# Performance work log

Measured on AMD Instinct MI355X. Metric: run time of the kernel, lower is better.

## Reference

```python
import jax, jax.numpy as jnp
import numpy as np

PI = float(np.pi)


def _mat(rows):
    # rows: 4 lists of 4 [..., ] arrays -> [..., 4, 4]
    return jnp.stack([jnp.stack(r, axis=-1) for r in rows], axis=-2)


def _local_frames(q):
    """q: [..., 7] joint angles -> list of 8 local [..., 4, 4] transforms."""
    z = jnp.zeros_like(q[..., 0])
    o = jnp.ones_like(z)

    def cs(a):
        return jnp.cos(a), jnp.sin(a)

    c0, s0 = cs(q[..., 0])
    c1, s1 = cs(q[..., 1])
    c2, s2 = cs(q[..., 2] - 0.5 * PI)
    c3, s3 = cs(q[..., 3])
    c4, s4 = cs(q[..., 4])
    c5, s5 = cs(q[..., 5] + 0.5 * PI)
    c6, s6 = cs(q[..., 6] - 0.5 * PI)

    m0 = _mat([[c0, -s0, z, z], [s0, c0, z, z], [z, z, o, z], [z, z, z, o]])
    m1 = _mat([[c1, -s1, z, z], [z, z, -o, z], [s1, c1, z, z], [z, z, z, o]])
    m2 = _mat([[c2, -s2, z, z], [z, z, o, 0.4 * o], [-s2, -c2, z, z], [z, z, z, o]])
    m3 = _mat([[c3, -s3, z, z], [z, z, -o, z], [s3, c3, z, z], [z, z, z, o]])
    m4 = _mat([[-c4, s4, z, z], [z, z, o, 0.39 * o], [s4, c4, z, z], [z, z, z, o]])
    m5 = _mat([[c5, -s5, z, z], [z, z, -o, z], [s5, c5, z, z], [z, z, z, o]])
    m6 = _mat([[c6, -s6, z, z], [z, z, -o, z], [s6, c6, z, z], [z, z, z, o]])
    m7 = _mat([[-o, z, z, z], [z, z, o, 0.118 * o], [z, o, z, z], [z, z, z, o]])
    return [m0, m1, m2, m3, m4, m5, m6, m7]


def setup_inputs() -> dict:
    key = jax.random.key(0)
    x = jax.random.normal(key, (2000000, 7), dtype=jnp.float32)
    return {"x": x}


def reference(x):
    mats = _local_frames(x)
    frames = [mats[0]]
    f = mats[0]
    for m in mats[1:]:  # fixed chain of 7 tiny 4x4 matmuls over batch
        f = jnp.einsum("...ij,...jk->...ik", f, m)
        frames.append(f)
    return jnp.stack(frames, axis=-3)  # [..., 8, 4, 4]
```

## Files before the change

### kernel.cpp

```cpp
#include <hip/hip_runtime.h>


#define GROUPS_PER_BLOCK 8
#define LSTRIDE 25

namespace {

struct V3 { float x, y, z; };
__device__ __forceinline__ V3 v3(float x, float y, float z) { return {x, y, z}; }

__device__ __forceinline__ void stage3(float4* p, V3 c0, V3 c1, V3 c2, V3 c3) {
    p[0] = make_float4(c0.x, c1.x, c2.x, c3.x);
    p[1] = make_float4(c0.y, c1.y, c2.y, c3.y);
    p[2] = make_float4(c0.z, c1.z, c2.z, c3.z);
}

__device__ __forceinline__ void compute_stage(const float* __restrict__ q,
                                              float4* __restrict__ buf,
                                              int lane, long long grp, long long n)
{
    long long i = grp * 64 + lane;
    if (i >= n) i = n - 1;
    const float* qi = q + i * 7;
    const float HPI = 1.57079632679489662f;

    float qv[7];
    #pragma unroll
    for (int k = 0; k < 7; ++k) qv[k] = qi[k];

    float c[7], s[7];
    __sincosf(qv[0], &s[0], &c[0]);
    __sincosf(qv[1], &s[1], &c[1]);
    __sincosf(qv[2] - HPI, &s[2], &c[2]);
    __sincosf(qv[3], &s[3], &c[3]);
    __sincosf(qv[4], &s[4], &c[4]);
    __sincosf(qv[5] + HPI, &s[5], &c[5]);
    __sincosf(qv[6] - HPI, &s[6], &c[6]);

    float4* myS = buf + lane * LSTRIDE;

    V3 f0 = v3(c[0], s[0], 0.f);
    V3 f1 = v3(-s[0], c[0], 0.f);
    V3 f2 = v3(0.f, 0.f, 1.f);
    V3 f3 = v3(0.f, 0.f, 0.f);

    #define TYPE_A(cc, ss)                                              \
        {                                                               \
            V3 t0 = v3((cc)*f0.x + (ss)*f2.x, (cc)*f0.y + (ss)*f2.y, (cc)*f0.z + (ss)*f2.z); \
            V3 t1 = v3((cc)*f2.x - (ss)*f0.x, (cc)*f2.y - (ss)*f0.y, (cc)*f2.z - (ss)*f0.z); \
            V3 t2 = v3(-f1.x, -f1.y, -f1.z);                            \
            f0 = t0; f1 = t1; f2 = t2;                                  \
        }

    stage3(myS + 0, f0, f1, f2, f3);

    TYPE_A(c[1], s[1]);
    stage3(myS + 3, f0, f1, f2, f3);

    {
        V3 t0 = v3(c[2]*f0.x - s[2]*f2.x, c[2]*f0.y - s[2]*f2.y, c[2]*f0.z - s[2]*f2.z);
        V3 t1 = v3(-(s[2]*f0.x + c[2]*f2.x), -(s[2]*f0.y + c[2]*f2.y), -(s[2]*f0.z + c[2]*f2.z));
        V3 t2 = f1;
        f3 = v3(0.4f*f1.x + f3.x, 0.4f*f1.y + f3.y, 0.4f*f1.z + f3.z);
        f0 = t0; f1 = t1; f2 = t2;
    }
    stage3(myS + 6, f0, f1, f2, f3);

    TYPE_A(c[3], s[3]);
    stage3(myS + 9, f0, f1, f2, f3);

    {
        V3 t0 = v3(s[4]*f2.x - c[4]*f0.x, s[4]*f2.y - c[4]*f0.y, s[4]*f2.z - c[4]*f0.z);
        V3 t1 = v3(s[4]*f0.x + c[4]*f2.x, s[4]*f0.y + c[4]*f2.y, s[4]*f0.z + c[4]*f2.z);
        V3 t2 = f1;
        f3 = v3(0.39f*f1.x + f3.x, 0.39f*f1.y + f3.y, 0.39f*f1.z + f3.z);
        f0 = t0; f1 = t1; f2 = t2;
    }
    stage3(myS + 12, f0, f1, f2, f3);

    TYPE_A(c[5], s[5]);
    stage3(myS + 15, f0, f1, f2, f3);

    TYPE_A(c[6], s[6]);
    stage3(myS + 18, f0, f1, f2, f3);

    {
        V3 t0 = v3(-f0.x, -f0.y, -f0.z);
        V3 t1 = f2;
        V3 t2 = f1;
        f3 = v3(0.118f*f1.x + f3.x, 0.118f*f1.y + f3.y, 0.118f*f1.z + f3.z);
        f0 = t0; f1 = t1; f2 = t2;
    }
    stage3(myS + 21, f0, f1, f2, f3);

    #undef TYPE_A
}

__device__ __forceinline__ void flush_group(const float4* __restrict__ buf,
                                            float4* __restrict__ out,
                                            int lane, long long grp, long long n,
                                            bool full)
{
    const int p  = lane & 31;
    const int eh = lane >> 5;
    const int f  = p >> 2;
    const int r  = p & 3;
    const int rr = (r == 3) ? 2 : r;
    const int base_off = eh * LSTRIDE + f * 3 + rr;
    const bool isr3 = (r == 3);
    float4* gb = out + grp * 2048;

    if (full) {
        #pragma unroll
        for (int j = 0; j < 32; ++j) {
            float4 v = buf[j * (2 * LSTRIDE) + base_off];
            if (isr3) v = make_float4(0.f, 0.f, 0.f, 1.f);
            gb[j * 64 + lane] = v;
        }
    } else {
        #pragma unroll
        for (int j = 0; j < 32; ++j) {
            float4 v = buf[j * (2 * LSTRIDE) + base_off];
            if (isr3) v = make_float4(0.f, 0.f, 0.f, 1.f);
            long long e = (long long)((j * 64 + lane) >> 5);
            if (grp * 64 + e < n) gb[j * 64 + lane] = v;
        }
    }
}

}

__global__ __launch_bounds__(64) void fk_chain_kernel(const float* __restrict__ q,
                                                      float4* __restrict__ out,
                                                      int n, int ngroups)
{
    __shared__ float4 lds[2][64 * LSTRIDE];

    const int lane = threadIdx.x;
    const long long g0 = (long long)blockIdx.x * GROUPS_PER_BLOCK;
    if (g0 >= ngroups) return;
    const int ng = (ngroups - g0 < GROUPS_PER_BLOCK) ? (int)(ngroups - g0)
                                                     : GROUPS_PER_BLOCK;

    compute_stage(q, lds[0], lane, g0, n);
    int cur = 0;
    for (int t = 1; t < ng; ++t) {
        __syncthreads();
        compute_stage(q, lds[cur ^ 1], lane, g0 + t, n);
        bool full = ((g0 + t - 1) * 64 + 64 <= (long long)n);
        flush_group(lds[cur], out, lane, g0 + t - 1, n, full);
        cur ^= 1;
    }
    __syncthreads();
    bool full = ((g0 + ng - 1) * 64 + 64 <= (long long)n);
    flush_group(lds[cur], out, lane, g0 + ng - 1, n, full);
}

extern "C" void kernel_launch(void* const* d_in, const int* in_sizes, int n_in,
                              void* d_out, int out_size, void* d_ws, size_t ws_size,
                              hipStream_t stream) {
    const float* x = (const float*)d_in[0];
    float* out = (float*)d_out;
    int n = in_sizes[0] / 7;
    int ngroups = (n + 63) >> 6;
    int grid = (ngroups + GROUPS_PER_BLOCK - 1) / GROUPS_PER_BLOCK;
    fk_chain_kernel<<<grid, 64, 0, stream>>>(x, (float4*)out, n, ngroups);
}
```

Before: 214.6 us.

## Process one 64-element group per block instead of double-buffered multi-group loop

Removes the per-block loop over 8 groups with a double-buffered LDS pipeline and instead launches one 64-thread block per 64-element group. Each block computes its transforms into a single LDS buffer, syncs once, and writes its coalesced output. This halves LDS per block, which may allow more resident blocks to hide latency, but it gives up the in-block overlap of compute and store and launches about 8x more blocks.

```diff
diff --git a/kernel.cpp b/kernel.cpp
--- a/kernel.cpp
+++ b/kernel.cpp
@@ -1,7 +1,6 @@
 #include <hip/hip_runtime.h>
 
 
-#define GROUPS_PER_BLOCK 8
 #define LSTRIDE 25
 
 namespace {
@@ -15,12 +14,19 @@
     p[2] = make_float4(c0.z, c1.z, c2.z, c3.z);
 }
 
-__device__ __forceinline__ void compute_stage(const float* __restrict__ q,
-                                              float4* __restrict__ buf,
-                                              int lane, long long grp, long long n)
+}
+
+__global__ __launch_bounds__(64) void fk_chain_kernel(const float* __restrict__ q,
+                                                      float4* __restrict__ out,
+                                                      int n)
 {
-    long long i = grp * 64 + lane;
+    __shared__ float4 lds[64 * LSTRIDE];
+
+    const int lane = threadIdx.x;
+    const long long e0 = (long long)blockIdx.x * 64;
+    long long i = e0 + lane;
     if (i >= n) i = n - 1;
+
     const float* qi = q + i * 7;
     const float HPI = 1.57079632679489662f;
 
@@ -37,7 +43,7 @@
     __sincosf(qv[5] + HPI, &s[5], &c[5]);
     __sincosf(qv[6] - HPI, &s[6], &c[6]);
 
-    float4* myS = buf + lane * LSTRIDE;
+    float4* myS = lds + lane * LSTRIDE;
 
     V3 f0 = v3(c[0], s[0], 0.f);
     V3 f1 = v3(-s[0], c[0], 0.f);
@@ -94,66 +100,34 @@
     stage3(myS + 21, f0, f1, f2, f3);
 
     #undef TYPE_A
-}
 
-__device__ __forceinline__ void flush_group(const float4* __restrict__ buf,
-                                            float4* __restrict__ out,
-                                            int lane, long long grp, long long n,
-                                            bool full)
-{
+    __syncthreads();
+
+    const int hi = lane >> 5;
     const int p  = lane & 31;
-    const int eh = lane >> 5;
-    const int f  = p >> 2;
+    const int fr = p >> 2;
     const int r  = p & 3;
-    const int rr = (r == 3) ? 2 : r;
-    const int base_off = eh * LSTRIDE + f * 3 + rr;
+    const int rb = hi * LSTRIDE + fr * 3 + ((r == 3) ? 2 : r);
     const bool isr3 = (r == 3);
-    float4* gb = out + grp * 2048;
+    const float4 row3 = make_float4(0.f, 0.f, 0.f, 1.f);
 
-    if (full) {
+    float4* gb = out + e0 * 32;
+    if (e0 + 64 <= (long long)n) {
         #pragma unroll
         for (int j = 0; j < 32; ++j) {
-            float4 v = buf[j * (2 * LSTRIDE) + base_off];
-            if (isr3) v = make_float4(0.f, 0.f, 0.f, 1.f);
+            float4 v = lds[j * (2 * LSTRIDE) + rb];
+            if (isr3) v = row3;
             gb[j * 64 + lane] = v;
         }
     } else {
         #pragma unroll
         for (int j = 0; j < 32; ++j) {
-            float4 v = buf[j * (2 * LSTRIDE) + base_off];
-            if (isr3) v = make_float4(0.f, 0.f, 0.f, 1.f);
-            long long e = (long long)((j * 64 + lane) >> 5);
-            if (grp * 64 + e < n) gb[j * 64 + lane] = v;
+            float4 v = lds[j * (2 * LSTRIDE) + rb];
+            if (isr3) v = row3;
+            if (e0 + (j * 2 + hi) < (long long)n)
+                gb[j * 64 + lane] = v;
         }
     }
-}
-
-}
-
-__global__ __launch_bounds__(64) void fk_chain_kernel(const float* __restrict__ q,
-                                                      float4* __restrict__ out,
-                                                      int n, int ngroups)
-{
-    __shared__ float4 lds[2][64 * LSTRIDE];
-
-    const int lane = threadIdx.x;
-    const long long g0 = (long long)blockIdx.x * GROUPS_PER_BLOCK;
-    if (g0 >= ngroups) return;
-    const int ng = (ngroups - g0 < GROUPS_PER_BLOCK) ? (int)(ngroups - g0)
-                                                     : GROUPS_PER_BLOCK;
-
-    compute_stage(q, lds[0], lane, g0, n);
-    int cur = 0;
-    for (int t = 1; t < ng; ++t) {
-        __syncthreads();
-        compute_stage(q, lds[cur ^ 1], lane, g0 + t, n);
-        bool full = ((g0 + t - 1) * 64 + 64 <= (long long)n);
-        flush_group(lds[cur], out, lane, g0 + t - 1, n, full);
-        cur ^= 1;
-    }
-    __syncthreads();
-    bool full = ((g0 + ng - 1) * 64 + 64 <= (long long)n);
-    flush_group(lds[cur], out, lane, g0 + ng - 1, n, full);
 }
 
 extern "C" void kernel_launch(void* const* d_in, const int* in_sizes, int n_in,
@@ -162,7 +136,6 @@
     const float* x = (const float*)d_in[0];
     float* out = (float*)d_out;
     int n = in_sizes[0] / 7;
-    int ngroups = (n + 63) >> 6;
-    int grid = (ngroups + GROUPS_PER_BLOCK - 1) / GROUPS_PER_BLOCK;
-    fk_chain_kernel<<<grid, 64, 0, stream>>>(x, (float4*)out, n, ngroups);
+    int grid = (n + 63) >> 6;
+    fk_chain_kernel<<<grid, 64, 0, stream>>>(x, (float4*)out, n);
 }
```

New measurement: 187.7 us, median of 2. 12.6% less time.
